# Kernel optimization log

Hardware: AMD Instinct MI355X
Metric: run time of the kernel (lower is better)

The kernel has to match this reference:

```python
import jax, jax.numpy as jnp
import numpy as np

NEG = -1e30  # finite stand-in for -inf to keep gradients NaN-free


def setup_inputs() -> dict:
    key = jax.random.key(0)
    k1, k2, k3 = jax.random.split(key, 3)
    T, B, V, L = 1600, 48, 1000, 128
    # acoustic model output: already log-softmax normalized, layout [T, B, V]
    logits = jax.random.normal(k1, (T, B, V), dtype=jnp.float32)
    log_probs = jax.nn.log_softmax(logits, axis=-1)
    # flat concatenated targets (nonzero labels; 0 is blank), uniform length L per utt
    targets = jax.random.randint(k2, (B * L,), 1, V, dtype=jnp.int32)
    input_lengths = jax.random.randint(k3, (B,), 3 * T // 4, T + 1, dtype=jnp.int32)
    target_lengths = jnp.full((B,), L, dtype=jnp.int32)
    return {
        "log_probs": log_probs,
        "targets": targets,
        "input_lengths": input_lengths,
        "target_lengths": target_lengths,
    }


def _ctc_neg_log_likelihood(log_probs, targets, input_lengths, target_lengths):
    """Exact log-semiring CTC forward (total score over all alignments),
    equivalent to k2.intersect_dense(ctc_topo o linear_fsa, dense) +
    get_tot_scores(log_semiring=True). Returns -sum_b log p(y_b | x_b).
    log_probs: [T, B, V]; targets: flat [B*L]; lengths: [B].
    """
    T, B, V = log_probs.shape
    L = targets.shape[0] // B
    tg = targets.reshape(B, L)
    S = 2 * L + 1  # blank-interleaved extended label sequence

    ext = jnp.zeros((B, S), dtype=jnp.int32).at[:, 1::2].set(tg)  # [B, S]
    # skip transition s-2 -> s allowed iff label[s] != blank and != label[s-2]
    allow_skip = jnp.concatenate(
        [jnp.zeros((B, 2), dtype=bool),
         (ext[:, 2:] != 0) & (ext[:, 2:] != ext[:, :-2])],
        axis=1,
    )

    def emit(lp_t):  # [B, V] -> [B, S]
        return jnp.take_along_axis(lp_t, ext, axis=1)

    e0 = emit(log_probs[0])
    alpha0 = jnp.full((B, S), NEG, dtype=log_probs.dtype)
    alpha0 = alpha0.at[:, 0].set(e0[:, 0]).at[:, 1].set(e0[:, 1])

    def step(alpha, xs):
        lp_t, t = xs
        prev1 = jnp.pad(alpha[:, :-1], ((0, 0), (1, 0)), constant_values=NEG)
        prev2 = jnp.pad(alpha[:, :-2], ((0, 0), (2, 0)), constant_values=NEG)
        a = jnp.logaddexp(alpha, prev1)
        a = jnp.where(allow_skip, jnp.logaddexp(a, prev2), a)
        new = a + emit(lp_t)
        # freeze alpha once past each utterance's input length
        alpha = jnp.where((t < input_lengths)[:, None], new, alpha)
        return alpha, None

    alpha, _ = jax.lax.scan(step, alpha0, (log_probs[1:], jnp.arange(1, T)))

    # all target_lengths are L, so the final states are S-1 (last blank) and S-2
    tot_scores = jnp.logaddexp(alpha[:, S - 1], alpha[:, S - 2])  # [B]
    return -jnp.sum(tot_scores)


def reference(log_probs, targets, input_lengths, target_lengths):
    return _ctc_neg_log_likelihood(log_probs, targets, input_lengths, target_lengths)
```

## Files before the change

kernel.cpp:

```cpp
#include <hip/hip_runtime.h>
#include <math.h>

#define TT 1600
#define BB 48
#define VV 1000
#define LL 128
#define EMS 132
#define EMTOT (TT*EMS)
#define TILE 60
#define TILEF (TILE*EMS)
#define NTILES 27

#define DPPF(x, ctrl) __int_as_float(__builtin_amdgcn_update_dpp( \
    0, __float_as_int(x), (ctrl), 0xf, 0xf, true))

__global__ __launch_bounds__(256) void ctc_gather_kernel(
    const float* __restrict__ lp,
    const int* __restrict__ targets,
    float* __restrict__ em)
{
  const int wv   = threadIdx.x >> 6;
  const int lane = threadIdx.x & 63;
  const int gw   = blockIdx.x * 4 + wv;
  const int b    = gw % BB;
  const int t0   = (gw / BB) * 4;

  const int* __restrict__ tg = targets + b * LL;
  const int g0 = (lane == 0) ? 0 : tg[lane - 1];
  const int g1 = tg[lane + 63];
  const int g2 = tg[127];
  const int p0 = (lane == 0) ? 0 : (lane + 1);
  const int p1 = lane + 65;

  float v0[4], v1[4], v2[4];
#pragma unroll
  for (int r = 0; r < 4; r++) {
    const float* row = lp + ((size_t)(t0 + r) * BB + b) * VV;
    v0[r] = row[g0];
    v1[r] = row[g1];
    if (lane == 0) v2[r] = row[g2];
  }
#pragma unroll
  for (int r = 0; r < 4; r++) {
    float* erow = em + (size_t)b * EMTOT + (size_t)(t0 + r) * EMS;
    erow[p0] = __expf(v0[r]);
    erow[p1] = __expf(v1[r]);
    if (lane == 0) erow[129] = __expf(v2[r]);
  }
}

__global__ __launch_bounds__(128) void ctc_dp_kernel(
    const float* __restrict__ em,
    const int* __restrict__ targets,
    const int* __restrict__ input_lengths,
    float* __restrict__ out)
{
  __shared__ float sbuf[2][TILEF];
  const int b    = blockIdx.x;
  const int lane = threadIdx.x & 63;
  const int wv   = threadIdx.x >> 6;
  const int NS   = input_lengths[b] - 1;
  const float* __restrict__ base = em + (size_t)b * EMTOT;

  float skip1 = 0.f, skip3 = 0.f, m63 = 0.f, sel1648 = 0.f, sel32 = 0.f;
  if (wv == 0) {
    const int* __restrict__ tg = targets + b * LL;
    const int c0  = tg[2 * lane];
    const int c1  = tg[2 * lane + 1];
    const int cm1 = (lane > 0) ? tg[2 * lane - 1] : c0;
    skip1   = (lane > 0 && c0 != cm1) ? 1.0f : 0.0f;
    skip3   = (c1 != c0) ? 1.0f : 0.0f;
    m63     = (lane == 63) ? 1.0f : 0.0f;
    sel1648 = (lane == 16 || lane == 48) ? 1.0f : 0.0f;
    sel32   = (lane == 32) ? 1.0f : 0.0f;
  }

  float a0 = 0.f, a1 = 0.f, a2 = 0.f, a3 = 0.f, a4 = 0.f;
  int esum = 0;
  float  pb_r[4];
  float2 ev_r[4];

#define STAGE(KN) do {                                               \
    const float4* src_ = (const float4*)(base + (size_t)(KN) * TILEF); \
    float* dst_ = sbuf[(KN) & 1];                                    \
    const int nf4_ = ((KN) == NTILES - 1) ? 1320 : 1980;             \
    _Pragma("unroll")                                                \
    for (int j = 0; j < 31; j++) {                                   \
      int idx_ = (j << 6) + lane;                                    \
      if (idx_ < nf4_)                                               \
        __builtin_amdgcn_global_load_lds(                            \
            (const __attribute__((address_space(1))) unsigned int*)(src_ + idx_), \
            (__attribute__((address_space(3))) unsigned int*)(dst_ + (j << 8)),   \
            16, 0, 0);                                               \
    }                                                                \
  } while (0)

#define STEP(PB, EV) do {                                            \
    float am1 = DPPF(a3, 0x111);                     \
    float h15 = DPPF(a3, 0x142);                    \
    float h31 = DPPF(a3, 0x143);                    \
    am1 = fmaf(sel1648, h15, am1);                                   \
    am1 = fmaf(sel32,   h31, am1);                                   \
    float s0 = a0 + am1;                                             \
    float s1 = fmaf(skip1, am1, a0 + a1);                            \
    float s2 = a1 + a2;                                              \
    float s3 = fmaf(skip3, a1, a2 + a3);                             \
    float s4 = fmaf(a3, m63, a4);                                    \
    a0 = s0 * (PB); a1 = s1 * (EV).x; a2 = s2 * (PB);                \
    a3 = s3 * (EV).y; a4 = s4 * (PB);                                \
  } while (0)

#define RESCALE() do {                                               \
    float mx = fmaxf(fmaxf(fmaxf(a0, a1), fmaxf(a2, a3)), a4);       \
    mx = fmaxf(mx, DPPF(mx, 0x111));                  \
    mx = fmaxf(mx, DPPF(mx, 0x112));                  \
    mx = fmaxf(mx, DPPF(mx, 0x114));                  \
    mx = fmaxf(mx, DPPF(mx, 0x118));                  \
    mx = fmaxf(mx, DPPF(mx, 0x142));                    \
    mx = fmaxf(mx, DPPF(mx, 0x143));      \
    int eb = (__builtin_amdgcn_readlane(__float_as_int(mx), 63) >> 23) & 0xFF; \
    int se = 157 - eb;                       \
    se = se < -126 ? -126 : (se > 127 ? 127 : se);                   \
    float sc = __uint_as_float((unsigned)(se + 127) << 23);          \
    a0 *= sc; a1 *= sc; a2 *= sc; a3 *= sc; a4 *= sc;                \
    esum -= se;                                                      \
  } while (0)

  if (wv == 1) STAGE(0);
  __syncthreads();

  for (int k = 0; k < NTILES; k++) {
    if (wv == 1) {
      if (k + 1 < NTILES) STAGE(k + 1);
    } else {
      const float* lb = sbuf[k & 1];
      if (k == 0 && lane == 0) { a0 = lb[0]; a1 = lb[2]; }
      int tbeg = (k == 0) ? 1 : k * TILE;
      int tend = k * TILE + TILE - 1;
      if (tend > NS) tend = NS;
      int n = tend - tbeg + 1;
      if (n > 0) {
        const float* lb0 = lb + (tbeg - k * TILE) * EMS;
        const float* lbe = lb0 + 2 + 2 * lane;
#define LOADSLOT(D, TF) do {                                         \
    int off_ = (TF) * EMS;                                           \
    pb_r[D] = lb0[off_];                                             \
    ev_r[D] = *(const float2*)(lbe + off_);                          \
  } while (0)
#pragma unroll
        for (int d = 0; d < 4; d++) { if (d < n) LOADSLOT(d, d); }
        int i = 0;
        while (i + 4 <= n) {
#pragma unroll
          for (int d = 0; d < 4; d++) {
            STEP(pb_r[d], ev_r[d]);
            int tf = i + 4 + d;
            if (tf < n) LOADSLOT(d, tf);
          }
          RESCALE();
          i += 4;
        }
#pragma unroll
        for (int d = 0; d < 3; d++) {
          if (i + d < n) STEP(pb_r[d], ev_r[d]);
        }
        if (i < n) RESCALE();
#undef LOADSLOT
      }
    }
    __syncthreads();
  }

  if (wv == 0 && lane == 63) {
    float tot = __logf(a3 + a4) + (float)esum * 0.69314718055994530942f;
    atomicAdd(out, -tot);
  }
#undef STEP
#undef RESCALE
#undef STAGE
}

extern "C" void kernel_launch(void* const* d_in, const int* in_sizes, int n_in,
                              void* d_out, int out_size, void* d_ws, size_t ws_size,
                              hipStream_t stream) {
  const float* lp            = (const float*)d_in[0];
  const int*   targets       = (const int*)d_in[1];
  const int*   input_lengths = (const int*)d_in[2];

  float* em  = (float*)d_ws;
  float* out = (float*)d_out;

  hipMemsetAsync(out, 0, sizeof(float), stream);

  ctc_gather_kernel<<<4800, 256, 0, stream>>>(lp, targets, em);
  ctc_dp_kernel<<<BB, 128, 0, stream>>>(em, targets, input_lengths, out);
}
```

Baseline: 563.3 us.

## Stage gather rows through LDS, widen DP staging waves, defer rescale

The gather kernel now loads 8 full contiguous vocab rows per block into LDS with global_load_lds, then gathers target emissions from shared memory instead of doing scattered global reads. The DP kernel grows to 256 threads so three waves share tile staging. The rescale is deferred: each group applies the previous group's scale factor, taking the max reduction off the recurrence's critical path. The gather now reads all of log_probs (~300MB) instead of only the target entries, trading more bandwidth for coalesced access.

```diff
diff --git a/kernel.cpp b/kernel.cpp
--- a/kernel.cpp
+++ b/kernel.cpp
@@ -14,42 +14,52 @@
 #define DPPF(x, ctrl) __int_as_float(__builtin_amdgcn_update_dpp( \
     0, __float_as_int(x), (ctrl), 0xf, 0xf, true))
 
+typedef const __attribute__((address_space(1))) unsigned int* gldlds_src_t;
+typedef __attribute__((address_space(3))) unsigned int*       gldlds_dst_t;
+
 __global__ __launch_bounds__(256) void ctc_gather_kernel(
     const float* __restrict__ lp,
     const int* __restrict__ targets,
     float* __restrict__ em)
 {
-  const int wv   = threadIdx.x >> 6;
-  const int lane = threadIdx.x & 63;
-  const int gw   = blockIdx.x * 4 + wv;
-  const int b    = gw % BB;
-  const int t0   = (gw / BB) * 4;
-
-  const int* __restrict__ tg = targets + b * LL;
-  const int g0 = (lane == 0) ? 0 : tg[lane - 1];
-  const int g1 = tg[lane + 63];
-  const int g2 = tg[127];
-  const int p0 = (lane == 0) ? 0 : (lane + 1);
-  const int p1 = lane + 65;
-
-  float v0[4], v1[4], v2[4];
-#pragma unroll
-  for (int r = 0; r < 4; r++) {
-    const float* row = lp + ((size_t)(t0 + r) * BB + b) * VV;
-    v0[r] = row[g0];
-    v1[r] = row[g1];
-    if (lane == 0) v2[r] = row[g2];
-  }
-#pragma unroll
-  for (int r = 0; r < 4; r++) {
-    float* erow = em + (size_t)b * EMTOT + (size_t)(t0 + r) * EMS;
-    erow[p0] = __expf(v0[r]);
-    erow[p1] = __expf(v1[r]);
-    if (lane == 0) erow[129] = __expf(v2[r]);
+  __shared__ float rb[8000];
+  const int tid  = threadIdx.x;
+  const int wv   = tid >> 6;
+  const int lane = tid & 63;
+  const size_t row0 = (size_t)blockIdx.x * 8;
+
+  const float4* src = (const float4*)(lp + row0 * VV);
+#pragma unroll
+  for (int i = 0; i < 8; i++) {
+    int idx = tid + (i << 8);
+    if (idx < 2000)
+      __builtin_amdgcn_global_load_lds(
+          (gldlds_src_t)(src + idx),
+          (gldlds_dst_t)(rb + ((size_t)((i << 8) + (wv << 6)) << 2)),
+          16, 0, 0);
+  }
+  __syncthreads();
+
+  const int t  = (int)(row0 / BB);
+  const int b0 = (int)(row0 % BB);
+#pragma unroll
+  for (int r = 0; r < 2; r++) {
+    const int bl = 2 * wv + r;
+    const int b  = b0 + bl;
+    const int* __restrict__ tg = targets + b * LL;
+    const float* row = rb + bl * 1000;
+    const int g0 = (lane == 0) ? 0 : tg[lane - 1];
+    const int g1 = tg[lane + 63];
+    float v0 = row[g0];
+    float v1 = row[g1];
+    float* erow = em + (size_t)b * EMTOT + (size_t)t * EMS;
+    erow[(lane == 0) ? 0 : (lane + 1)] = __expf(v0);
+    erow[lane + 65] = __expf(v1);
+    if (lane == 0) erow[129] = __expf(row[tg[127]]);
   }
 }
 
-__global__ __launch_bounds__(128) void ctc_dp_kernel(
+__global__ __launch_bounds__(256) void ctc_dp_kernel(
     const float* __restrict__ em,
     const int* __restrict__ targets,
     const int* __restrict__ input_lengths,
@@ -77,6 +87,8 @@
 
   float a0 = 0.f, a1 = 0.f, a2 = 0.f, a3 = 0.f, a4 = 0.f;
   int esum = 0;
+  float sc_p = 1.0f;
+  int   se_p = 0;
   float  pb_r[4];
   float2 ev_r[4];
 
@@ -84,21 +96,19 @@
     const float4* src_ = (const float4*)(base + (size_t)(KN) * TILEF); \
     float* dst_ = sbuf[(KN) & 1];                                    \
     const int nf4_ = ((KN) == NTILES - 1) ? 1320 : 1980;             \
-    _Pragma("unroll")                                                \
-    for (int j = 0; j < 31; j++) {                                   \
+    for (int j = wv - 1; j < 31; j += 3) {                           \
       int idx_ = (j << 6) + lane;                                    \
       if (idx_ < nf4_)                                               \
         __builtin_amdgcn_global_load_lds(                            \
-            (const __attribute__((address_space(1))) unsigned int*)(src_ + idx_), \
-            (__attribute__((address_space(3))) unsigned int*)(dst_ + (j << 8)),   \
-            16, 0, 0);                                               \
+            (gldlds_src_t)(src_ + idx_),                             \
+            (gldlds_dst_t)(dst_ + (j << 8)), 16, 0, 0);              \
     }                                                                \
   } while (0)
 
 #define STEP(PB, EV) do {                                            \
-    float am1 = DPPF(a3, 0x111);                     \
-    float h15 = DPPF(a3, 0x142);                    \
-    float h31 = DPPF(a3, 0x143);                    \
+    float am1 = DPPF(a3, 0x111);                                     \
+    float h15 = DPPF(a3, 0x142);                                     \
+    float h31 = DPPF(a3, 0x143);                                     \
     am1 = fmaf(sel1648, h15, am1);                                   \
     am1 = fmaf(sel32,   h31, am1);                                   \
     float s0 = a0 + am1;                                             \
@@ -110,27 +120,28 @@
     a3 = s3 * (EV).y; a4 = s4 * (PB);                                \
   } while (0)
 
-#define RESCALE() do {                                               \
+#define RESCALE_DEFERRED() do {                                      \
+    a0 *= sc_p; a1 *= sc_p; a2 *= sc_p; a3 *= sc_p; a4 *= sc_p;      \
+    esum -= se_p;                                                    \
     float mx = fmaxf(fmaxf(fmaxf(a0, a1), fmaxf(a2, a3)), a4);       \
-    mx = fmaxf(mx, DPPF(mx, 0x111));                  \
-    mx = fmaxf(mx, DPPF(mx, 0x112));                  \
-    mx = fmaxf(mx, DPPF(mx, 0x114));                  \
-    mx = fmaxf(mx, DPPF(mx, 0x118));                  \
-    mx = fmaxf(mx, DPPF(mx, 0x142));                    \
-    mx = fmaxf(mx, DPPF(mx, 0x143));      \
+    mx = fmaxf(mx, DPPF(mx, 0x111));                                 \
+    mx = fmaxf(mx, DPPF(mx, 0x112));                                 \
+    mx = fmaxf(mx, DPPF(mx, 0x114));                                 \
+    mx = fmaxf(mx, DPPF(mx, 0x118));                                 \
+    mx = fmaxf(mx, DPPF(mx, 0x142));                                 \
+    mx = fmaxf(mx, DPPF(mx, 0x143));          \
     int eb = (__builtin_amdgcn_readlane(__float_as_int(mx), 63) >> 23) & 0xFF; \
-    int se = 157 - eb;                       \
+    int se = 157 - eb;                         \
     se = se < -126 ? -126 : (se > 127 ? 127 : se);                   \
-    float sc = __uint_as_float((unsigned)(se + 127) << 23);          \
-    a0 *= sc; a1 *= sc; a2 *= sc; a3 *= sc; a4 *= sc;                \
-    esum -= se;                                                      \
-  } while (0)
-
-  if (wv == 1) STAGE(0);
+    sc_p = __uint_as_float((unsigned)(se + 127) << 23);              \
+    se_p = se;                                                       \
+  } while (0)
+
+  if (wv) STAGE(0);
   __syncthreads();
 
   for (int k = 0; k < NTILES; k++) {
-    if (wv == 1) {
+    if (wv) {
       if (k + 1 < NTILES) STAGE(k + 1);
     } else {
       const float* lb = sbuf[k & 1];
@@ -157,14 +168,13 @@
             int tf = i + 4 + d;
             if (tf < n) LOADSLOT(d, tf);
           }
-          RESCALE();
+          RESCALE_DEFERRED();
           i += 4;
         }
 #pragma unroll
         for (int d = 0; d < 3; d++) {
           if (i + d < n) STEP(pb_r[d], ev_r[d]);
         }
-        if (i < n) RESCALE();
 #undef LOADSLOT
       }
     }
@@ -172,11 +182,12 @@
   }
 
   if (wv == 0 && lane == 63) {
+    a3 *= sc_p; a4 *= sc_p; esum -= se_p;
     float tot = __logf(a3 + a4) + (float)esum * 0.69314718055994530942f;
     atomicAdd(out, -tot);
   }
 #undef STEP
-#undef RESCALE
+#undef RESCALE_DEFERRED
 #undef STAGE
 }
 
@@ -192,6 +203,6 @@
 
   hipMemsetAsync(out, 0, sizeof(float), stream);
 
-  ctc_gather_kernel<<<4800, 256, 0, stream>>>(lp, targets, em);
-  ctc_dp_kernel<<<BB, 128, 0, stream>>>(em, targets, input_lengths, out);
+  ctc_gather_kernel<<<(TT * BB) / 8, 256, 0, stream>>>(lp, targets, em);
+  ctc_dp_kernel<<<BB, 256, 0, stream>>>(em, targets, input_lengths, out);
 }
```

Measured after the change: 557.5 us. No clear change (-1.0%).
